# Optimization experiments

Measured on AMD Instinct MI355X. Metric: run time of the kernel, lower is better.

The kernel has to match this reference:

```python
import jax, jax.numpy as jnp
import numpy as np

V, H, NH, I, L, P = 32000, 1024, 16, 4096, 8, 2048
B, S = 2, 2048
DH = H // NH
EPS = 1e-5


def setup_inputs() -> dict:
    key = jax.random.key(0)
    ks = jax.random.split(key, 12)
    std = 0.02
    inp = {
        'input_ids': jax.random.randint(ks[0], (B, S), 0, V),
        'attention_mask': jnp.ones((B, S), dtype=jnp.float32),
        'tok_emb': jax.random.normal(ks[1], (V, H), jnp.float32) * std,
        'pos_emb': jax.random.normal(ks[2], (P, H), jnp.float32) * std,
        # per-layer params stacked on leading L dim (torch Linear convention: y = x @ W.T + b)
        'Wq': jax.random.normal(ks[3], (L, H, H), jnp.float32) * std,
        'bq': jnp.zeros((L, H), jnp.float32),
        'Wk': jax.random.normal(ks[4], (L, H, H), jnp.float32) * std,
        'bk': jnp.zeros((L, H), jnp.float32),
        'Wv': jax.random.normal(ks[5], (L, H, H), jnp.float32) * std,
        'bv': jnp.zeros((L, H), jnp.float32),
        'Wi': jax.random.normal(ks[6], (L, I, H), jnp.float32) * std,
        'bi': jnp.zeros((L, I), jnp.float32),
        'Wo': jax.random.normal(ks[7], (L, H, I), jnp.float32) * std,
        'bo': jnp.zeros((L, H), jnp.float32),
        'ln1_g': jnp.ones((L, H), jnp.float32),
        'ln1_b': jnp.zeros((L, H), jnp.float32),
        'ln2_g': jnp.ones((L, H), jnp.float32),
        'ln2_b': jnp.zeros((L, H), jnp.float32),
        'lnf_g': jnp.ones((H,), jnp.float32),
        'lnf_b': jnp.zeros((H,), jnp.float32),
        'Wlm': jax.random.normal(ks[8], (V, H), jnp.float32) * std,
    }
    return inp


def _layer_norm(x, g, b):
    m = jnp.mean(x, axis=-1, keepdims=True)
    v = jnp.var(x, axis=-1, keepdims=True)
    return (x - m) * jax.lax.rsqrt(v + EPS) * g + b


def reference(input_ids, attention_mask, tok_emb, pos_emb, Wq, bq, Wk, bk, Wv, bv,
              Wi, bi, Wo, bo, ln1_g, ln1_b, ln2_g, ln2_b, lnf_g, lnf_b, Wlm):
    b, s = input_ids.shape
    h = tok_emb[input_ids] + pos_emb[jnp.arange(s)][None, :, :]  # [B,S,H]
    mask = (1.0 - attention_mask)[:, None, None, :] * -10000.0   # [B,1,1,S]
    scale = 1.0 / (DH ** 0.5)

    def split_heads(x):  # [B,S,H] -> [B,NH,S,DH]
        return x.reshape(b, s, NH, DH).transpose(0, 2, 1, 3)

    def block(h, p):
        wq, bq_, wk, bk_, wv, bv_, wi, bi_, wo, bo_, g1, b1, g2, b2 = p
        q = split_heads(h @ wq.T + bq_)
        k = split_heads(h @ wk.T + bk_)
        v = split_heads(h @ wv.T + bv_)
        scores = jnp.einsum('bhqd,bhkd->bhqk', q, k) * scale + mask
        probs = jax.nn.softmax(scores, axis=-1)
        ctx = jnp.einsum('bhqk,bhkd->bhqd', probs, v)
        ctx = ctx.transpose(0, 2, 1, 3).reshape(b, s, H)
        h1 = _layer_norm(h + ctx, g1, b1)
        mlp = jax.nn.gelu(h1 @ wi.T + bi_, approximate=False) @ wo.T + bo_
        return _layer_norm(h1 + mlp, g2, b2), None

    h, _ = jax.lax.scan(block, h, (Wq, bq, Wk, bk, Wv, bv, Wi, bi, Wo, bo,
                                   ln1_g, ln1_b, ln2_g, ln2_b))
    h = _layer_norm(h, lnf_g, lnf_b)
    return h @ Wlm.T  # [B,S,V]
```

## Files before the change

### kernel.cpp

```cpp
#include <hip/hip_runtime.h>
#include <hip/hip_bf16.h>

#define V_ 32000
#define H_ 1024
#define NH_ 16
#define I_ 4096
#define L_ 8
#define B_ 2
#define S_ 2048
#define DH_ 64
#define M_ 4096
#define QS_ 3072

typedef __attribute__((ext_vector_type(4))) float f32x4;
typedef __attribute__((ext_vector_type(8))) short s16x8;

#define BARRIER() do { asm volatile("" ::: "memory"); __builtin_amdgcn_s_barrier(); asm volatile("" ::: "memory"); } while (0)
#define SCHEDB()  __builtin_amdgcn_sched_barrier(0)

__device__ __forceinline__ unsigned short f2b(float f) {
  union { float f; unsigned u; } x; x.f = f;
  return (unsigned short)((x.u + 0x7FFFu + ((x.u >> 16) & 1u)) >> 16);
}

__device__ __forceinline__ void gl_lds16(const unsigned short* g, unsigned short* l) {
  __builtin_amdgcn_global_load_lds(
      (__attribute__((address_space(1))) const void*)g,
      (__attribute__((address_space(3))) void*)l, 16, 0, 0);
}

__global__ __launch_bounds__(256) void wcvt(const float* __restrict__ src,
                                            unsigned short* __restrict__ dst) {
  size_t i = ((size_t)blockIdx.x * 256 + threadIdx.x) * 4;
  float4 v = *(const float4*)(src + i);
  ushort4 b;
  b.x = f2b(v.x); b.y = f2b(v.y); b.z = f2b(v.z); b.w = f2b(v.w);
  *(ushort4*)(dst + i) = b;
}

__global__ __launch_bounds__(256) void qkvcat_all(const float* __restrict__ q,
                                                  const float* __restrict__ k,
                                                  const float* __restrict__ v,
                                                  unsigned short* __restrict__ dst) {
  size_t i = ((size_t)blockIdx.x * 256 + threadIdx.x) * 4;
  size_t l = i / (3u * H_ * H_);
  size_t r = i - l * (3u * H_ * H_);
  const float* s; size_t off;
  if (r < (size_t)H_ * H_)          { s = q; off = l * H_ * H_ + r; }
  else if (r < 2u * H_ * H_)        { s = k; off = l * H_ * H_ + r - (size_t)H_ * H_; }
  else                              { s = v; off = l * H_ * H_ + r - 2u * H_ * H_; }
  float4 vv = *(const float4*)(s + off);
  ushort4 b;
  b.x = f2b(vv.x); b.y = f2b(vv.y); b.z = f2b(vv.z); b.w = f2b(vv.w);
  *(ushort4*)(dst + i) = b;
}

__global__ __launch_bounds__(256) void qkvcat(const float* __restrict__ q,
                                              const float* __restrict__ k,
                                              const float* __restrict__ v,
                                              unsigned short* __restrict__ dst) {
  int i = (blockIdx.x * 256 + threadIdx.x) * 4;
  const float* s; int off;
  if (i < H_ * H_)          { s = q; off = i; }
  else if (i < 2 * H_ * H_) { s = k; off = i - H_ * H_; }
  else                      { s = v; off = i - 2 * H_ * H_; }
  float4 vv = *(const float4*)(s + off);
  ushort4 b;
  b.x = f2b(vv.x); b.y = f2b(vv.y); b.z = f2b(vv.z); b.w = f2b(vv.w);
  *(ushort4*)(dst + i) = b;
}

__global__ __launch_bounds__(256) void bcat(const float* __restrict__ bq,
                                            const float* __restrict__ bk,
                                            const float* __restrict__ bv,
                                            float* __restrict__ dst) {
  int i = blockIdx.x * 256 + threadIdx.x;
  int l = i / (3 * H_), r = i - l * 3 * H_;
  int p = r >> 10, c = r & (H_ - 1);
  const float* s = (p == 0) ? bq : ((p == 1) ? bk : bv);
  dst[i] = s[l * H_ + c];
}

__global__ __launch_bounds__(256) void embed_kernel(
    const int* __restrict__ ids, const float* __restrict__ tok,
    const float* __restrict__ pos, float* __restrict__ h,
    unsigned short* __restrict__ xbf)
{
  int row = blockIdx.x;
  int c4 = threadIdx.x;
  int id = ids[row];
  int s = row & (S_ - 1);
  float4 tv = ((const float4*)(tok + (size_t)id * H_))[c4];
  float4 pv = ((const float4*)(pos + (size_t)s * H_))[c4];
  float4 v; v.x = tv.x + pv.x; v.y = tv.y + pv.y; v.z = tv.z + pv.z; v.w = tv.w + pv.w;
  ((float4*)(h + (size_t)row * H_))[c4] = v;
  ushort4 b; b.x = f2b(v.x); b.y = f2b(v.y); b.z = f2b(v.z); b.w = f2b(v.w);
  ((ushort4*)(xbf + (size_t)row * H_))[c4] = b;
}

template<int EPI>
__global__ __launch_bounds__(256) void gemm_bt(
    const unsigned short* __restrict__ A, const unsigned short* __restrict__ Wb,
    const float* __restrict__ bias, float* __restrict__ outf,
    unsigned short* __restrict__ outb, int M, int N, int K)
{
  __shared__ unsigned short As[2][128][32];
  __shared__ unsigned short Bs[2][128][32];
  int t = threadIdx.x;
  int lane = t & 63, wid = t >> 6;
  int m0 = blockIdx.x * 128, n0 = blockIdx.y * 128;
  int wm = (wid >> 1) * 64, wn = (wid & 1) * 64;
  int fr = lane & 15, hi = lane >> 4;
  int lrow = lane >> 2;
  int lcolsw = (((lane & 3) ^ (lrow & 3)) * 8);
  int ke = ((hi ^ (fr & 3)) * 8);

  f32x4 acc[4][4] = {};

  const unsigned short* Abase = A  + (size_t)(m0 + wid * 32 + lrow) * K + lcolsw;
  const unsigned short* Bbase = Wb + (size_t)(n0 + wid * 32 + lrow) * K + lcolsw;

  auto stage = [&](int s, int k0) {
    gl_lds16(Abase + k0,                  &As[s][wid * 32][0]);
    gl_lds16(Abase + k0 + (size_t)16 * K, &As[s][wid * 32 + 16][0]);
    gl_lds16(Bbase + k0,                  &Bs[s][wid * 32][0]);
    gl_lds16(Bbase + k0 + (size_t)16 * K, &Bs[s][wid * 32 + 16][0]);
  };

  stage(0, 0);

  int cur = 0;
  for (int k0 = 0; k0 < K; k0 += 32) {
    asm volatile("s_waitcnt vmcnt(0)" ::: "memory");
    BARRIER();
    if (k0 + 32 < K) stage(cur ^ 1, k0 + 32);
    SCHEDB();
    s16x8 af[4], bfr[4];
    #pragma unroll
    for (int i = 0; i < 4; ++i) af[i]  = *(const s16x8*)(&As[cur][wm + i * 16 + fr][ke]);
    #pragma unroll
    for (int j = 0; j < 4; ++j) bfr[j] = *(const s16x8*)(&Bs[cur][wn + j * 16 + fr][ke]);
    #pragma unroll
    for (int i = 0; i < 4; ++i)
      #pragma unroll
      for (int j = 0; j < 4; ++j)
        acc[i][j] = __builtin_amdgcn_mfma_f32_16x16x32_bf16(af[i], bfr[j], acc[i][j], 0, 0, 0);
    cur ^= 1;
  }

  int fq = lane >> 4;
  #pragma unroll
  for (int i = 0; i < 4; ++i) {
    #pragma unroll
    for (int j = 0; j < 4; ++j) {
      #pragma unroll
      for (int r = 0; r < 4; ++r) {
        int row = m0 + wm + i * 16 + fq * 4 + r;
        int col = n0 + wn + j * 16 + fr;
        float v = acc[i][j][r] + (bias ? bias[col] : 0.f);
        if (EPI == 0) {
          outf[(size_t)row * N + col] = v;
        } else if (EPI == 1) {
          float ge = 0.5f * v * (1.0f + erff(v * 0.70710678118f));
          outb[(size_t)row * N + col] = f2b(ge);
        } else {
          outb[(size_t)row * N + col] = f2b(v);
        }
      }
    }
  }
}

template<int EPI>
__global__ __launch_bounds__(512, 2) void gemm256(
    const unsigned short* __restrict__ A, const unsigned short* __restrict__ Wb,
    const float* __restrict__ bias, float* __restrict__ outf,
    unsigned short* __restrict__ outb, int M, int N, int K)
{
  __shared__ unsigned short ASm[2][16384];
  __shared__ unsigned short BSm[2][16384];

  const int t = threadIdx.x;
  const int lane = t & 63, wid = t >> 6;
  const int wm = wid >> 2, wn = wid & 3;
  const int fr = lane & 15, hi = lane >> 4;

  const int Nt = N >> 8;
  const int nwg = gridDim.x;
  const int cpx = nwg >> 3;
  int bid = (int)blockIdx.x;
  int swz = (bid & 7) * cpx + (bid >> 3);
  int band = swz / (4 * Nt);
  int rem = swz - band * (4 * Nt);
  const int m0 = (band * 4 + (rem & 3)) << 8;
  const int n0 = (rem >> 2) << 8;

  const int NT = K >> 6;

  const int srow = lane >> 3;
  const int scol = ((lane & 7) ^ srow) << 3;
  const int ch0 = wid * 2;

  const int axorb = (fr & 7) << 4;
  const int koe0 = ((hi * 16) ^ axorb) >> 1;
  const int koe1 = (((hi * 16) | 64) ^ axorb) >> 1;

  f32x4 acc[8][4] = {};

  auto stage_half = [&](int slot, int h, int k0) {
    if (h < 2) {
      const unsigned short* src =
          A + (size_t)(m0 + h * 128 + ch0 * 8 + srow) * K + k0 + scol;
      unsigned short* dst = &ASm[slot][(h * 128 + ch0 * 8) * 64];
      gl_lds16(src, dst);
      gl_lds16(src + (size_t)8 * K, dst + 8 * 64);
    } else {
      const unsigned short* src =
          Wb + (size_t)(n0 + (h - 2) * 128 + ch0 * 8 + srow) * K + k0 + scol;
      unsigned short* dst = &BSm[slot][((h - 2) * 128 + ch0 * 8) * 64];
      gl_lds16(src, dst);
      gl_lds16(src + (size_t)8 * K, dst + 8 * 64);
    }
  };

  stage_half(0, 2, 0); stage_half(0, 3, 0); stage_half(0, 0, 0); stage_half(0, 1, 0);

  s16x8 af0[4][2], af1[4][2], bfv[4][2];

  for (int T = 0; T < NT; ++T) {
    const int s = T & 1;
    const int k1 = (T + 1) << 6;
    const bool more = (T + 1 < NT);

    asm volatile("s_waitcnt vmcnt(0)" ::: "memory");
    BARRIER();
    if (more) {
      stage_half(s ^ 1, 2, k1); stage_half(s ^ 1, 3, k1);
      stage_half(s ^ 1, 0, k1); stage_half(s ^ 1, 1, k1);
    }
    SCHEDB();

    const unsigned short* As_ = ASm[s];
    const unsigned short* Bs_ = BSm[s];

    #pragma unroll
    for (int mi = 0; mi < 4; ++mi) {
      const unsigned short* p = As_ + (wm * 128 + mi * 16 + fr) * 64;
      af0[mi][0] = *(const s16x8*)(p + koe0);
      af0[mi][1] = *(const s16x8*)(p + koe1);
    }
    #pragma unroll
    for (int nj = 0; nj < 4; ++nj) {
      const unsigned short* p = Bs_ + (wn * 64 + nj * 16 + fr) * 64;
      bfv[nj][0] = *(const s16x8*)(p + koe0);
      bfv[nj][1] = *(const s16x8*)(p + koe1);
    }
    SCHEDB();
    __builtin_amdgcn_s_setprio(1);
    #pragma unroll
    for (int mi = 0; mi < 4; ++mi)
      #pragma unroll
      for (int nj = 0; nj < 2; ++nj) {
        acc[mi][nj] = __builtin_amdgcn_mfma_f32_16x16x32_bf16(af0[mi][0], bfv[nj][0], acc[mi][nj], 0, 0, 0);
        acc[mi][nj] = __builtin_amdgcn_mfma_f32_16x16x32_bf16(af0[mi][1], bfv[nj][1], acc[mi][nj], 0, 0, 0);
      }
    __builtin_amdgcn_s_setprio(0);
    SCHEDB();

    #pragma unroll
    for (int mi = 0; mi < 4; ++mi) {
      const unsigned short* p = As_ + (wm * 128 + (mi + 4) * 16 + fr) * 64;
      af1[mi][0] = *(const s16x8*)(p + koe0);
      af1[mi][1] = *(const s16x8*)(p + koe1);
    }
    SCHEDB();
    __builtin_amdgcn_s_setprio(1);
    #pragma unroll
    for (int mi = 0; mi < 4; ++mi)
      #pragma unroll
      for (int nj = 2; nj < 4; ++nj) {
        acc[mi][nj] = __builtin_amdgcn_mfma_f32_16x16x32_bf16(af0[mi][0], bfv[nj][0], acc[mi][nj], 0, 0, 0);
        acc[mi][nj] = __builtin_amdgcn_mfma_f32_16x16x32_bf16(af0[mi][1], bfv[nj][1], acc[mi][nj], 0, 0, 0);
      }
    __builtin_amdgcn_s_setprio(0);
    SCHEDB();

    __builtin_amdgcn_s_setprio(1);
    #pragma unroll
    for (int mi = 0; mi < 4; ++mi)
      #pragma unroll
      for (int nj = 2; nj < 4; ++nj) {
        acc[mi + 4][nj] = __builtin_amdgcn_mfma_f32_16x16x32_bf16(af1[mi][0], bfv[nj][0], acc[mi + 4][nj], 0, 0, 0);
        acc[mi + 4][nj] = __builtin_amdgcn_mfma_f32_16x16x32_bf16(af1[mi][1], bfv[nj][1], acc[mi + 4][nj], 0, 0, 0);
      }
    __builtin_amdgcn_s_setprio(0);
    SCHEDB();

    __builtin_amdgcn_s_setprio(1);
    #pragma unroll
    for (int mi = 0; mi < 4; ++mi)
      #pragma unroll
      for (int nj = 0; nj < 2; ++nj) {
        acc[mi + 4][nj] = __builtin_amdgcn_mfma_f32_16x16x32_bf16(af1[mi][0], bfv[nj][0], acc[mi + 4][nj], 0, 0, 0);
        acc[mi + 4][nj] = __builtin_amdgcn_mfma_f32_16x16x32_bf16(af1[mi][1], bfv[nj][1], acc[mi + 4][nj], 0, 0, 0);
      }
    __builtin_amdgcn_s_setprio(0);
  }

  #pragma unroll
  for (int mi = 0; mi < 8; ++mi) {
    #pragma unroll
    for (int nj = 0; nj < 4; ++nj) {
      #pragma unroll
      for (int r = 0; r < 4; ++r) {
        int row = m0 + wm * 128 + mi * 16 + hi * 4 + r;
        int col = n0 + wn * 64 + nj * 16 + fr;
        float v = acc[mi][nj][r] + (bias ? bias[col] : 0.f);
        if (EPI == 0) {
          outf[(size_t)row * N + col] = v;
        } else if (EPI == 1) {
          float ge = 0.5f * v * (1.0f + erff(v * 0.70710678118f));
          outb[(size_t)row * N + col] = f2b(ge);
        } else {
          outb[(size_t)row * N + col] = f2b(v);
        }
      }
    }
  }
}

__global__ __launch_bounds__(256) void transpose_v_bf16(
    const unsigned short* __restrict__ v, unsigned short* __restrict__ vT)
{
  __shared__ unsigned short tile[32][34];
  int bh = blockIdx.z;
  int b = bh >> 4, hh = bh & 15;
  const unsigned short* src = v + (size_t)b * S_ * QS_ + hh * DH_;
  unsigned short* dst = vT + (size_t)bh * DH_ * S_;
  int s0 = blockIdx.x * 32, d0 = blockIdx.y * 32;
  int x = threadIdx.x, y = threadIdx.y;
  #pragma unroll
  for (int i = 0; i < 4; ++i)
    tile[y + i * 8][x] = src[(size_t)(s0 + y + i * 8) * QS_ + d0 + x];
  __syncthreads();
  #pragma unroll
  for (int i = 0; i < 4; ++i)
    dst[(size_t)(d0 + y + i * 8) * S_ + s0 + x] = tile[x][y + i * 8];
}

#define KB_ 64
#define SPL_ 1024
__global__ __launch_bounds__(512) void flash_mfma(
    const unsigned short* __restrict__ qb,
    const unsigned short* __restrict__ kb,
    const unsigned short* __restrict__ vtb,
    const float* __restrict__ mask,
    float* __restrict__ opart,
    float2* __restrict__ ml)
{
  __shared__ unsigned short K2[2][KB_ * DH_];
  __shared__ unsigned short V2[2][DH_ * KB_];
  __shared__ unsigned short Ps[8][16][72];
  __shared__ float xpose[8][16];

  const float LOG2E = 1.4426950408889634f;
  const float SCL = 0.125f * LOG2E;
  int t = threadIdx.x, lane = t & 63, wid = t >> 6;
  int blk = blockIdx.x;
  int bh = blk & 31;
  int rest = blk >> 5;
  int qt = rest & 15, sp = rest >> 4;
  int b = bh >> 4, hh = bh & 15;
  int row0 = b * S_ + qt * 128 + wid * 16;
  int fr = lane & 15, hi = lane >> 4;
  const float* mrow = mask + (size_t)b * S_;
  const int kv0 = sp * SPL_;

  s16x8 qf[2];
  {
    const unsigned short* qrow = qb + (size_t)(row0 + fr) * QS_ + hh * DH_;
    qf[0] = *(const s16x8*)(qrow + hi * 8);
    qf[1] = *(const s16x8*)(qrow + 32 + hi * 8);
  }

  float m_run = -3.0e38f, l_run = 0.f;
  f32x4 octx[4] = {};

  const unsigned short* Kbase = kb + (size_t)b * S_ * QS_ + hh * DH_;
  const unsigned short* Vbase = vtb + (size_t)bh * DH_ * S_;

  int crow = lane >> 3;
  int scol = ((lane & 7) ^ crow) * 8;

  auto stage = [&](int slot, int t0) {
    gl_lds16(Kbase + (size_t)(t0 + wid * 8 + crow) * QS_ + scol, &K2[slot][wid * 512]);
    gl_lds16(Vbase + (size_t)(wid * 8 + crow) * S_ + t0 + scol,  &V2[slot][wid * 512]);
  };

  stage(0, kv0);

  const int swz = (fr & 7) * 8;

  int tt = 0;
  for (int t0 = kv0; t0 < kv0 + SPL_; t0 += KB_, ++tt) {
    int slot = tt & 1;
    __syncthreads();
    if (t0 + KB_ < kv0 + SPL_) stage(slot ^ 1, t0 + KB_);

    f32x4 sacc[4] = {};
    #pragma unroll
    for (int g = 0; g < 4; ++g) {
      #pragma unroll
      for (int i = 0; i < 2; ++i) {
        s16x8 kf = *(const s16x8*)(&K2[slot][(g * 16 + fr) * 64 + ((i * 32 + hi * 8) ^ swz)]);
        sacc[g] = __builtin_amdgcn_mfma_f32_16x16x32_bf16(kf, qf[i], sacc[g], 0, 0, 0);
      }
    }

    float sc[4][4];
    float tm = -3.0e38f;
    #pragma unroll
    for (int g = 0; g < 4; ++g) {
      float4 mq = *(const float4*)(mrow + t0 + g * 16 + hi * 4);
      #pragma unroll
      for (int r = 0; r < 4; ++r) {
        float mk = (1.0f - ((const float*)&mq)[r]) * (-10000.0f * LOG2E);
        float v = sacc[g][r] * SCL + mk;
        sc[g][r] = v;
        tm = fmaxf(tm, v);
      }
    }
    tm = fmaxf(tm, __shfl_xor(tm, 16));
    tm = fmaxf(tm, __shfl_xor(tm, 32));

    if (!__all(tm <= m_run + 8.0f)) {
      float mn = fmaxf(m_run, tm);
      float corr = exp2f(m_run - mn);
      m_run = mn; l_run *= corr;
      xpose[wid][fr] = corr;
      float cr0 = xpose[wid][hi * 4 + 0];
      float cr1 = xpose[wid][hi * 4 + 1];
      float cr2 = xpose[wid][hi * 4 + 2];
      float cr3 = xpose[wid][hi * 4 + 3];
      #pragma unroll
      for (int dg = 0; dg < 4; ++dg) {
        octx[dg][0] *= cr0; octx[dg][1] *= cr1;
        octx[dg][2] *= cr2; octx[dg][3] *= cr3;
      }
    }

    float ps = 0.f;
    #pragma unroll
    for (int g = 0; g < 4; ++g)
      #pragma unroll
      for (int r = 0; r < 4; ++r) {
        float p = exp2f(sc[g][r] - m_run);
        sc[g][r] = p;
        ps += p;
      }
    ps += __shfl_xor(ps, 16);
    ps += __shfl_xor(ps, 32);
    l_run += ps;

    #pragma unroll
    for (int g = 0; g < 4; ++g) {
      uint2 pk;
      pk.x = (unsigned)f2b(sc[g][0]) | ((unsigned)f2b(sc[g][1]) << 16);
      pk.y = (unsigned)f2b(sc[g][2]) | ((unsigned)f2b(sc[g][3]) << 16);
      *(uint2*)(&Ps[wid][fr][g * 16 + hi * 4]) = pk;
    }

    #pragma unroll
    for (int kc = 0; kc < 2; ++kc) {
      s16x8 pf = *(const s16x8*)(&Ps[wid][fr][kc * 32 + hi * 8]);
      #pragma unroll
      for (int dg = 0; dg < 4; ++dg) {
        s16x8 vf2 = *(const s16x8*)(&V2[slot][(dg * 16 + fr) * 64 + ((kc * 32 + hi * 8) ^ swz)]);
        octx[dg] = __builtin_amdgcn_mfma_f32_16x16x32_bf16(pf, vf2, octx[dg], 0, 0, 0);
      }
    }
  }

  float* ob = opart + (size_t)sp * M_ * H_;
  #pragma unroll
  for (int dg = 0; dg < 4; ++dg) {
    size_t base = (size_t)(row0 + hi * 4) * H_ + hh * DH_ + dg * 16 + fr;
    ob[base]          = octx[dg][0];
    ob[base + H_]     = octx[dg][1];
    ob[base + 2 * H_] = octx[dg][2];
    ob[base + 3 * H_] = octx[dg][3];
  }
  if (hi == 0)
    ml[((size_t)sp * 32 + bh) * S_ + qt * 128 + wid * 16 + fr] =
        make_float2(m_run, l_run);
}

__global__ __launch_bounds__(256) void flash_merge(
    const float* __restrict__ o0, const float* __restrict__ o1,
    const float2* __restrict__ ml, float* __restrict__ ctx)
{
  int row = blockIdx.x, t = threadIdx.x;
  int hh = t >> 4;
  int bh = (row >> 11) * NH_ + hh;
  int q = row & (S_ - 1);
  float2 a = ml[(size_t)bh * S_ + q];
  float2 c = ml[(size_t)(32 + bh) * S_ + q];
  float m = fmaxf(a.x, c.x);
  float w0 = exp2f(a.x - m), w1 = exp2f(c.x - m);
  float inv = 1.0f / (a.y * w0 + c.y * w1);
  float4 v0 = ((const float4*)(o0 + (size_t)row * H_))[t];
  float4 v1 = ((const float4*)(o1 + (size_t)row * H_))[t];
  float4 o;
  o.x = (v0.x * w0 + v1.x * w1) * inv;
  o.y = (v0.y * w0 + v1.y * w1) * inv;
  o.z = (v0.z * w0 + v1.z * w1) * inv;
  o.w = (v0.w * w0 + v1.w * w1) * inv;
  ((float4*)(ctx + (size_t)row * H_))[t] = o;
}

__global__ __launch_bounds__(256) void add_ln(
    const float* __restrict__ x, const float* __restrict__ y,
    const float* __restrict__ g, const float* __restrict__ bb,
    float* __restrict__ outf, unsigned short* __restrict__ outb)
{
  __shared__ float a1[4], a2[4];
  int row = blockIdx.x, t = threadIdx.x;
  float4 v = ((const float4*)(x + (size_t)row * H_))[t];
  if (y) {
    float4 u = ((const float4*)(y + (size_t)row * H_))[t];
    v.x += u.x; v.y += u.y; v.z += u.z; v.w += u.w;
  }
  float s1 = v.x + v.y + v.z + v.w;
  float s2 = v.x * v.x + v.y * v.y + v.z * v.z + v.w * v.w;
  #pragma unroll
  for (int d = 32; d; d >>= 1) { s1 += __shfl_xor(s1, d); s2 += __shfl_xor(s2, d); }
  if ((t & 63) == 0) { a1[t >> 6] = s1; a2[t >> 6] = s2; }
  __syncthreads();
  s1 = a1[0] + a1[1] + a1[2] + a1[3];
  s2 = a2[0] + a2[1] + a2[2] + a2[3];
  float mean = s1 * (1.0f / H_);
  float var = s2 * (1.0f / H_) - mean * mean;
  float inv = rsqrtf(var + 1e-5f);
  float4 gv = ((const float4*)g)[t];
  float4 bv = ((const float4*)bb)[t];
  float4 o;
  o.x = (v.x - mean) * inv * gv.x + bv.x;
  o.y = (v.y - mean) * inv * gv.y + bv.y;
  o.z = (v.z - mean) * inv * gv.z + bv.z;
  o.w = (v.w - mean) * inv * gv.w + bv.w;
  if (outf) ((float4*)(outf + (size_t)row * H_))[t] = o;
  if (outb) {
    ushort4 ob; ob.x = f2b(o.x); ob.y = f2b(o.y); ob.z = f2b(o.z); ob.w = f2b(o.w);
    ((ushort4*)(outb + (size_t)row * H_))[t] = ob;
  }
}

extern "C" void kernel_launch(void* const* d_in, const int* in_sizes, int n_in,
                              void* d_out, int out_size, void* d_ws, size_t ws_size,
                              hipStream_t stream) {
  const int*   ids  = (const int*)d_in[0];
  const float* mask = (const float*)d_in[1];
  const float* tok  = (const float*)d_in[2];
  const float* pos  = (const float*)d_in[3];
  const float* Wq   = (const float*)d_in[4];
  const float* bq   = (const float*)d_in[5];
  const float* Wk   = (const float*)d_in[6];
  const float* bk   = (const float*)d_in[7];
  const float* Wv   = (const float*)d_in[8];
  const float* bv   = (const float*)d_in[9];
  const float* Wi   = (const float*)d_in[10];
  const float* bi   = (const float*)d_in[11];
  const float* Wo   = (const float*)d_in[12];
  const float* bo   = (const float*)d_in[13];
  const float* ln1g = (const float*)d_in[14];
  const float* ln1b = (const float*)d_in[15];
  const float* ln2g = (const float*)d_in[16];
  const float* ln2b = (const float*)d_in[17];
  const float* lnfg = (const float*)d_in[18];
  const float* lnfb = (const float*)d_in[19];
  const float* Wlm  = (const float*)d_in[20];
  float* out = (float*)d_out;

  char* w = (char*)d_ws;
  size_t off = 0;
  auto alloc = [&](size_t bytes) { void* p = w + off; off = (off + bytes + 255) & ~(size_t)255; return p; };
  float* h     = (float*)alloc((size_t)M_ * H_ * 4);
  float* ctxb  = (float*)alloc((size_t)M_ * H_ * 4);
  unsigned short* qkvb  = (unsigned short*)alloc((size_t)M_ * QS_ * 2);
  unsigned short* vtb   = (unsigned short*)alloc((size_t)B_ * NH_ * DH_ * S_ * 2);
  unsigned short* xbf   = (unsigned short*)alloc((size_t)M_ * H_ * 2);
  unsigned short* midbf = (unsigned short*)alloc((size_t)M_ * I_ * 2);
  float* bqkv  = (float*)alloc((size_t)L_ * QS_ * 4);
  float* opart = (float*)alloc((size_t)2 * M_ * H_ * 4);
  float2* mlbuf = (float2*)alloc((size_t)2 * 32 * S_ * 8);

  size_t wqkv_b = (size_t)L_ * 3 * H_ * H_ * 2;
  size_t wi_bb  = (size_t)L_ * I_ * H_ * 2;
  size_t wo_bb  = (size_t)L_ * H_ * I_ * 2;
  size_t wlm_bb = (size_t)V_ * H_ * 2;
  bool big = (ws_size - off) >= (wqkv_b + wi_bb + wo_bb + wlm_bb + 4 * 256);

  unsigned short *wqkv, *wi_a, *wo_a, *wlm_a, *wbuf = nullptr;
  if (big) {
    wqkv  = (unsigned short*)alloc(wqkv_b);
    wi_a  = (unsigned short*)alloc(wi_bb);
    wo_a  = (unsigned short*)alloc(wo_bb);
    wlm_a = (unsigned short*)alloc(wlm_bb);
    qkvcat_all<<<dim3((unsigned)((size_t)L_ * 3 * H_ * H_ / 1024)), 256, 0, stream>>>(Wq, Wk, Wv, wqkv);
    wcvt<<<dim3((unsigned)((size_t)L_ * I_ * H_ / 1024)), 256, 0, stream>>>(Wi, wi_a);
    wcvt<<<dim3((unsigned)((size_t)L_ * H_ * I_ / 1024)), 256, 0, stream>>>(Wo, wo_a);
    wcvt<<<dim3((unsigned)((size_t)V_ * H_ / 1024)), 256, 0, stream>>>(Wlm, wlm_a);
  } else {
    wbuf = (unsigned short*)alloc((size_t)V_ * H_ * 2);
  }

  bcat<<<dim3(L_ * QS_ / 256), 256, 0, stream>>>(bq, bk, bv, bqkv);
  embed_kernel<<<dim3(M_), 256, 0, stream>>>(ids, tok, pos, h, xbf);

  for (int l = 0; l < L_; ++l) {
    const unsigned short* wq_l;
    if (big) wq_l = wqkv + (size_t)l * 3 * H_ * H_;
    else {
      qkvcat<<<dim3(3 * H_ * H_ / 1024), 256, 0, stream>>>(
          Wq + (size_t)l * H_ * H_, Wk + (size_t)l * H_ * H_, Wv + (size_t)l * H_ * H_, wbuf);
      wq_l = wbuf;
    }
    gemm_bt<2><<<dim3(M_ / 128, QS_ / 128), 256, 0, stream>>>(
        xbf, wq_l, bqkv + (size_t)l * QS_, nullptr, qkvb, M_, QS_, H_);

    transpose_v_bf16<<<dim3(S_ / 32, DH_ / 32, B_ * NH_), dim3(32, 8), 0, stream>>>(
        qkvb + 2 * H_, vtb);
    flash_mfma<<<dim3(B_ * NH_ * S_ / 128 * 2), 512, 0, stream>>>(
        qkvb, qkvb + H_, vtb, mask, opart, mlbuf);
    flash_merge<<<dim3(M_), 256, 0, stream>>>(
        opart, opart + (size_t)M_ * H_, mlbuf, ctxb);

    add_ln<<<dim3(M_), 256, 0, stream>>>(h, ctxb, ln1g + l * H_, ln1b + l * H_, h, xbf);

    const unsigned short* wi_l;
    if (big) wi_l = wi_a + (size_t)l * I_ * H_;
    else {
      wcvt<<<dim3(I_ * H_ / 1024), 256, 0, stream>>>(Wi + (size_t)l * I_ * H_, wbuf);
      wi_l = wbuf;
    }
    gemm256<1><<<dim3((M_ / 256) * (I_ / 256)), 512, 0, stream>>>(
        xbf, wi_l, bi + l * I_, nullptr, midbf, M_, I_, H_);

    const unsigned short* wo_l;
    if (big) wo_l = wo_a + (size_t)l * H_ * I_;
    else {
      wcvt<<<dim3(H_ * I_ / 1024), 256, 0, stream>>>(Wo + (size_t)l * H_ * I_, wbuf);
      wo_l = wbuf;
    }
    gemm_bt<0><<<dim3(M_ / 128, H_ / 128), 256, 0, stream>>>(
        midbf, wo_l, bo + l * H_, ctxb, nullptr, M_, H_, I_);

    add_ln<<<dim3(M_), 256, 0, stream>>>(h, ctxb, ln2g + l * H_, ln2b + l * H_, h, xbf);
  }

  add_ln<<<dim3(M_), 256, 0, stream>>>(h, nullptr, lnfg, lnfb, nullptr, xbf);
  const unsigned short* wlm_l;
  if (big) wlm_l = wlm_a;
  else {
    wcvt<<<dim3(V_ * H_ / 1024), 256, 0, stream>>>(Wlm, wbuf);
    wlm_l = wbuf;
  }
  gemm256<0><<<dim3((M_ / 256) * (V_ / 256)), 512, 0, stream>>>(
      xbf, wlm_l, nullptr, out, nullptr, M_, V_, H_);
}
```

Baseline: 3.267 ms.

## Split-K the MLP down-projection, fuse flash merge into LayerNorm, interleave GEMM staging

The Wo GEMM (K=4096) gets split-K by two via blockIdx.z, writing two partial outputs into opart that the following add_ln sums. Its grid previously had only 256 blocks. The flash-attention merge is folded into the first residual+LayerNorm kernel, which removes one launch and the ctx round trip through global memory. In gemm256 the prefetch of the next K tile is spread between the MFMA groups instead of issued all at once after the barrier. Costs are extra partial-sum traffic for split-K and possible LDS/VMEM contention from the interleaved staging.

Result: faster. 2.919 ms (-10.6%).

```diff
diff --git a/kernel.cpp b/kernel.cpp
--- a/kernel.cpp
+++ b/kernel.cpp
@@ -102,13 +102,17 @@
 __global__ __launch_bounds__(256) void gemm_bt(
     const unsigned short* __restrict__ A, const unsigned short* __restrict__ Wb,
     const float* __restrict__ bias, float* __restrict__ outf,
-    unsigned short* __restrict__ outb, int M, int N, int K)
+    unsigned short* __restrict__ outb, int M, int N, int K, int ksz)
 {
   __shared__ unsigned short As[2][128][32];
   __shared__ unsigned short Bs[2][128][32];
   int t = threadIdx.x;
   int lane = t & 63, wid = t >> 6;
   int m0 = blockIdx.x * 128, n0 = blockIdx.y * 128;
+  int z = blockIdx.z;
+  int koff = z * ksz;
+  const float* bz = (z == 0) ? bias : nullptr;
+  if (EPI == 0) outf += (size_t)z * M * N;
   int wm = (wid >> 1) * 64, wn = (wid & 1) * 64;
   int fr = lane & 15, hi = lane >> 4;
   int lrow = lane >> 2;
@@ -127,13 +131,13 @@
     gl_lds16(Bbase + k0 + (size_t)16 * K, &Bs[s][wid * 32 + 16][0]);
   };
 
-  stage(0, 0);
+  stage(0, koff);
 
   int cur = 0;
-  for (int k0 = 0; k0 < K; k0 += 32) {
+  for (int k0 = koff; k0 < koff + ksz; k0 += 32) {
     asm volatile("s_waitcnt vmcnt(0)" ::: "memory");
     BARRIER();
-    if (k0 + 32 < K) stage(cur ^ 1, k0 + 32);
+    if (k0 + 32 < koff + ksz) stage(cur ^ 1, k0 + 32);
     SCHEDB();
     s16x8 af[4], bfr[4];
     #pragma unroll
@@ -157,7 +161,7 @@
       for (int r = 0; r < 4; ++r) {
         int row = m0 + wm + i * 16 + fq * 4 + r;
         int col = n0 + wn + j * 16 + fr;
-        float v = acc[i][j][r] + (bias ? bias[col] : 0.f);
+        float v = acc[i][j][r] + (bz ? bz[col] : 0.f);
         if (EPI == 0) {
           outf[(size_t)row * N + col] = v;
         } else if (EPI == 1) {
@@ -234,11 +238,6 @@
 
     asm volatile("s_waitcnt vmcnt(0)" ::: "memory");
     BARRIER();
-    if (more) {
-      stage_half(s ^ 1, 2, k1); stage_half(s ^ 1, 3, k1);
-      stage_half(s ^ 1, 0, k1); stage_half(s ^ 1, 1, k1);
-    }
-    SCHEDB();
 
     const unsigned short* As_ = ASm[s];
     const unsigned short* Bs_ = BSm[s];
@@ -255,6 +254,7 @@
       bfv[nj][0] = *(const s16x8*)(p + koe0);
       bfv[nj][1] = *(const s16x8*)(p + koe1);
     }
+    if (more) stage_half(s ^ 1, 2, k1);
     SCHEDB();
     __builtin_amdgcn_s_setprio(1);
     #pragma unroll
@@ -273,6 +273,7 @@
       af1[mi][0] = *(const s16x8*)(p + koe0);
       af1[mi][1] = *(const s16x8*)(p + koe1);
     }
+    if (more) stage_half(s ^ 1, 3, k1);
     SCHEDB();
     __builtin_amdgcn_s_setprio(1);
     #pragma unroll
@@ -285,6 +286,8 @@
     __builtin_amdgcn_s_setprio(0);
     SCHEDB();
 
+    if (more) stage_half(s ^ 1, 0, k1);
+    SCHEDB();
     __builtin_amdgcn_s_setprio(1);
     #pragma unroll
     for (int mi = 0; mi < 4; ++mi)
@@ -296,6 +299,8 @@
     __builtin_amdgcn_s_setprio(0);
     SCHEDB();
 
+    if (more) stage_half(s ^ 1, 1, k1);
+    SCHEDB();
     __builtin_amdgcn_s_setprio(1);
     #pragma unroll
     for (int mi = 0; mi < 4; ++mi)
@@ -495,10 +500,13 @@
         make_float2(m_run, l_run);
 }
 
-__global__ __launch_bounds__(256) void flash_merge(
-    const float* __restrict__ o0, const float* __restrict__ o1,
-    const float2* __restrict__ ml, float* __restrict__ ctx)
+__global__ __launch_bounds__(256) void add_ln_mrg(
+    const float* __restrict__ x, const float* __restrict__ o0,
+    const float* __restrict__ o1, const float2* __restrict__ ml,
+    const float* __restrict__ g, const float* __restrict__ bb,
+    float* __restrict__ outf, unsigned short* __restrict__ outb)
 {
+  __shared__ float a1[4], a2[4];
   int row = blockIdx.x, t = threadIdx.x;
   int hh = t >> 4;
   int bh = (row >> 11) * NH_ + hh;
@@ -507,19 +515,42 @@
   float2 c = ml[(size_t)(32 + bh) * S_ + q];
   float m = fmaxf(a.x, c.x);
   float w0 = exp2f(a.x - m), w1 = exp2f(c.x - m);
-  float inv = 1.0f / (a.y * w0 + c.y * w1);
-  float4 v0 = ((const float4*)(o0 + (size_t)row * H_))[t];
-  float4 v1 = ((const float4*)(o1 + (size_t)row * H_))[t];
+  float inv0 = 1.0f / (a.y * w0 + c.y * w1);
+  float4 v  = ((const float4*)(x  + (size_t)row * H_))[t];
+  float4 u0 = ((const float4*)(o0 + (size_t)row * H_))[t];
+  float4 u1 = ((const float4*)(o1 + (size_t)row * H_))[t];
+  v.x += (u0.x * w0 + u1.x * w1) * inv0;
+  v.y += (u0.y * w0 + u1.y * w1) * inv0;
+  v.z += (u0.z * w0 + u1.z * w1) * inv0;
+  v.w += (u0.w * w0 + u1.w * w1) * inv0;
+  float s1 = v.x + v.y + v.z + v.w;
+  float s2 = v.x * v.x + v.y * v.y + v.z * v.z + v.w * v.w;
+  #pragma unroll
+  for (int d = 32; d; d >>= 1) { s1 += __shfl_xor(s1, d); s2 += __shfl_xor(s2, d); }
+  if ((t & 63) == 0) { a1[t >> 6] = s1; a2[t >> 6] = s2; }
+  __syncthreads();
+  s1 = a1[0] + a1[1] + a1[2] + a1[3];
+  s2 = a2[0] + a2[1] + a2[2] + a2[3];
+  float mean = s1 * (1.0f / H_);
+  float var = s2 * (1.0f / H_) - mean * mean;
+  float inv = rsqrtf(var + 1e-5f);
+  float4 gv = ((const float4*)g)[t];
+  float4 bv = ((const float4*)bb)[t];
   float4 o;
-  o.x = (v0.x * w0 + v1.x * w1) * inv;
-  o.y = (v0.y * w0 + v1.y * w1) * inv;
-  o.z = (v0.z * w0 + v1.z * w1) * inv;
-  o.w = (v0.w * w0 + v1.w * w1) * inv;
-  ((float4*)(ctx + (size_t)row * H_))[t] = o;
+  o.x = (v.x - mean) * inv * gv.x + bv.x;
+  o.y = (v.y - mean) * inv * gv.y + bv.y;
+  o.z = (v.z - mean) * inv * gv.z + bv.z;
+  o.w = (v.w - mean) * inv * gv.w + bv.w;
+  if (outf) ((float4*)(outf + (size_t)row * H_))[t] = o;
+  if (outb) {
+    ushort4 ob; ob.x = f2b(o.x); ob.y = f2b(o.y); ob.z = f2b(o.z); ob.w = f2b(o.w);
+    ((ushort4*)(outb + (size_t)row * H_))[t] = ob;
+  }
 }
 
 __global__ __launch_bounds__(256) void add_ln(
     const float* __restrict__ x, const float* __restrict__ y,
+    const float* __restrict__ y2,
     const float* __restrict__ g, const float* __restrict__ bb,
     float* __restrict__ outf, unsigned short* __restrict__ outb)
 {
@@ -528,6 +559,10 @@
   float4 v = ((const float4*)(x + (size_t)row * H_))[t];
   if (y) {
     float4 u = ((const float4*)(y + (size_t)row * H_))[t];
+    v.x += u.x; v.y += u.y; v.z += u.z; v.w += u.w;
+  }
+  if (y2) {
+    float4 u = ((const float4*)(y2 + (size_t)row * H_))[t];
     v.x += u.x; v.y += u.y; v.z += u.z; v.w += u.w;
   }
   float s1 = v.x + v.y + v.z + v.w;
@@ -585,7 +620,6 @@
   size_t off = 0;
   auto alloc = [&](size_t bytes) { void* p = w + off; off = (off + bytes + 255) & ~(size_t)255; return p; };
   float* h     = (float*)alloc((size_t)M_ * H_ * 4);
-  float* ctxb  = (float*)alloc((size_t)M_ * H_ * 4);
   unsigned short* qkvb  = (unsigned short*)alloc((size_t)M_ * QS_ * 2);
   unsigned short* vtb   = (unsigned short*)alloc((size_t)B_ * NH_ * DH_ * S_ * 2);
   unsigned short* xbf   = (unsigned short*)alloc((size_t)M_ * H_ * 2);
@@ -625,17 +659,17 @@
           Wq + (size_t)l * H_ * H_, Wk + (size_t)l * H_ * H_, Wv + (size_t)l * H_ * H_, wbuf);
       wq_l = wbuf;
     }
-    gemm_bt<2><<<dim3(M_ / 128, QS_ / 128), 256, 0, stream>>>(
-        xbf, wq_l, bqkv + (size_t)l * QS_, nullptr, qkvb, M_, QS_, H_);
+    gemm_bt<2><<<dim3(M_ / 128, QS_ / 128, 1), 256, 0, stream>>>(
+        xbf, wq_l, bqkv + (size_t)l * QS_, nullptr, qkvb, M_, QS_, H_, H_);
 
     transpose_v_bf16<<<dim3(S_ / 32, DH_ / 32, B_ * NH_), dim3(32, 8), 0, stream>>>(
         qkvb + 2 * H_, vtb);
     flash_mfma<<<dim3(B_ * NH_ * S_ / 128 * 2), 512, 0, stream>>>(
         qkvb, qkvb + H_, vtb, mask, opart, mlbuf);
-    flash_merge<<<dim3(M_), 256, 0, stream>>>(
-        opart, opart + (size_t)M_ * H_, mlbuf, ctxb);
-
-    add_ln<<<dim3(M_), 256, 0, stream>>>(h, ctxb, ln1g + l * H_, ln1b + l * H_, h, xbf);
+
+    add_ln_mrg<<<dim3(M_), 256, 0, stream>>>(
+        h, opart, opart + (size_t)M_ * H_, mlbuf,
+        ln1g + l * H_, ln1b + l * H_, h, xbf);
 
     const unsigned short* wi_l;
     if (big) wi_l = wi_a + (size_t)l * I_ * H_;
@@ -652,13 +686,15 @@
       wcvt<<<dim3(H_ * I_ / 1024), 256, 0, stream>>>(Wo + (size_t)l * H_ * I_, wbuf);
       wo_l = wbuf;
     }
-    gemm_bt<0><<<dim3(M_ / 128, H_ / 128), 256, 0, stream>>>(
-        midbf, wo_l, bo + l * H_, ctxb, nullptr, M_, H_, I_);
-
-    add_ln<<<dim3(M_), 256, 0, stream>>>(h, ctxb, ln2g + l * H_, ln2b + l * H_, h, xbf);
-  }
-
-  add_ln<<<dim3(M_), 256, 0, stream>>>(h, nullptr, lnfg, lnfb, nullptr, xbf);
+    gemm_bt<0><<<dim3(M_ / 128, H_ / 128, 2), 256, 0, stream>>>(
+        midbf, wo_l, bo + l * H_, opart, nullptr, M_, H_, I_, I_ / 2);
+
+    add_ln<<<dim3(M_), 256, 0, stream>>>(
+        h, opart, opart + (size_t)M_ * H_,
+        ln2g + l * H_, ln2b + l * H_, h, xbf);
+  }
+
+  add_ln<<<dim3(M_), 256, 0, stream>>>(h, nullptr, nullptr, lnfg, lnfb, nullptr, xbf);
   const unsigned short* wlm_l;
   if (big) wlm_l = wlm_a;
   else {
```
